# Kernel tuning notes

Measured on AMD Instinct MI355X. Metric: run time of the kernel, lower is better.

The kernel has to match this reference:

```python
import jax, jax.numpy as jnp
import numpy as np

N_NODES = 50000
N_EDGES = 800000
IN_CH = 64
HID = 128
OUT_CH = 1
NUM_LAYERS = 3
NUM_TIMESTEPS = 3
EDGE_DIM = 25
NUM_GRAPHS = 1024
NEG = 0.01  # leaky_relu negative slope (torch default & GATConv arg)


def leaky(v):
    return jnp.where(v >= 0, v, NEG * v)


def seg_softmax(a, idx, n):
    # PyG softmax: exp(a - max_per_segment) / (sum_per_segment + 1e-16)
    m = jax.ops.segment_max(a, idx, num_segments=n)
    m = jnp.where(jnp.isfinite(m), m, 0.0)  # guard empty segments
    e = jnp.exp(a - m[idx])
    s = jax.ops.segment_sum(e, idx, num_segments=n)
    return e / (s[idx] + 1e-16)


def gru(inp, h, Wih, Whh, bih, bhh):
    gi = inp @ Wih.T + bih
    gh = h @ Whh.T + bhh
    ir, iz, inn = jnp.split(gi, 3, axis=-1)
    hr, hz, hn = jnp.split(gh, 3, axis=-1)
    r = jax.nn.sigmoid(ir + hr)
    z = jax.nn.sigmoid(iz + hz)
    n = jnp.tanh(inn + r * hn)
    return (1.0 - z) * n + z * h


def setup_inputs() -> dict:
    key = jax.random.key(0)
    ks = iter(jax.random.split(key, 40))

    def nrm(shape, s=0.05):
        return jax.random.normal(next(ks), shape, dtype=jnp.float32) * s

    L = NUM_LAYERS - 1
    H3 = 3 * HID
    inp = dict(
        x=jax.random.normal(next(ks), (N_NODES, IN_CH), dtype=jnp.float32),
        edge_index=jax.random.randint(next(ks), (2, N_EDGES), 0, N_NODES),
        batch=jnp.sort(jax.random.randint(next(ks), (N_NODES,), 0, NUM_GRAPHS)),
        W1=nrm((HID, IN_CH)), b1=jnp.zeros((HID,), jnp.float32),
        Wg1=nrm((HID, HID + EDGE_DIM)), att_l=nrm((HID,)), att_r=nrm((HID,)),
        Wg2=nrm((HID, HID)), bg=jnp.zeros((HID,), jnp.float32),
        Wih0=nrm((H3, HID)), Whh0=nrm((H3, HID)),
        bih0=jnp.zeros((H3,), jnp.float32), bhh0=jnp.zeros((H3,), jnp.float32),
        Wa=nrm((L, HID, HID)), att_src_a=nrm((L, HID)), att_dst_a=nrm((L, HID)),
        ba=jnp.zeros((L, HID), jnp.float32),
        Wih_a=nrm((L, H3, HID)), Whh_a=nrm((L, H3, HID)),
        bih_a=jnp.zeros((L, H3), jnp.float32), bhh_a=jnp.zeros((L, H3), jnp.float32),
        Wm=nrm((HID, HID)), att_src_m=nrm((HID,)), att_dst_m=nrm((HID,)),
        bm=jnp.zeros((HID,), jnp.float32),
        Wih_m=nrm((H3, HID)), Whh_m=nrm((H3, HID)),
        bih_m=jnp.zeros((H3,), jnp.float32), bhh_m=jnp.zeros((H3,), jnp.float32),
        W2=nrm((OUT_CH, HID)), b2=jnp.zeros((OUT_CH,), jnp.float32),
    )
    return inp


def reference(x, edge_index, batch, W1, b1, Wg1, att_l, att_r, Wg2, bg,
              Wih0, Whh0, bih0, bhh0, Wa, att_src_a, att_dst_a, ba,
              Wih_a, Whh_a, bih_a, bhh_a, Wm, att_src_m, att_dst_m, bm,
              Wih_m, Whh_m, bih_m, bhh_m, W2, b2):
    N = x.shape[0]
    E = edge_index.shape[1]
    src, dst = edge_index[0], edge_index[1]  # j -> i, aggregate at i=dst
    edge_attr = jnp.ones((E, EDGE_DIM), dtype=x.dtype)  # built inside original forward

    x = leaky(x @ W1.T + b1)

    # GATEConv: edge-feature-aware attention, sum aggregation
    xe = leaky(jnp.concatenate([x[src], edge_attr], axis=-1) @ Wg1.T)  # [E, H]
    a = seg_softmax(leaky(xe @ att_l + (x @ att_r)[dst]), dst, N)
    msg = (x[src] @ Wg2.T) * a[:, None]
    h = jax.nn.elu(jax.ops.segment_sum(msg, dst, num_segments=N) + bg)
    x = jax.nn.relu(gru(h, x, Wih0, Whh0, bih0, bhh0))

    # (num_layers - 1) GATConv + GRU atom updates
    for l in range(NUM_LAYERS - 1):
        xt = x @ Wa[l].T
        a = seg_softmax(leaky((xt @ att_src_a[l])[src] + (xt @ att_dst_a[l])[dst]), dst, N)
        h = jax.nn.elu(jax.ops.segment_sum(xt[src] * a[:, None], dst, num_segments=N) + ba[l])
        x = jax.nn.relu(gru(h, x, Wih_a[l], Whh_a[l], bih_a[l], bhh_a[l]))

    # attentive readout: bipartite GATConv node->molecule over num_timesteps
    out = jax.nn.relu(jax.ops.segment_sum(x, batch, num_segments=NUM_GRAPHS))
    xt = x @ Wm.T                 # shared lin for src (fixed across timesteps)
    a_src = xt @ att_src_m        # [N]
    for _ in range(NUM_TIMESTEPS):
        ot = out @ Wm.T           # shared lin for dst
        a = seg_softmax(leaky(a_src + (ot @ att_dst_m)[batch]), batch, NUM_GRAPHS)
        h = jax.nn.elu(jax.ops.segment_sum(xt * a[:, None], batch, num_segments=NUM_GRAPHS) + bm)
        out = jax.nn.relu(gru(h, out, Wih_m, Whh_m, bih_m, bhh_m))

    return out @ W2.T + b2
```

## Files before the change

### kernel.cpp

```cpp
#include <hip/hip_runtime.h>
#include <math.h>

#define NN 50000
#define NE 800000
#define NG 1024
#define HID 128

typedef __attribute__((ext_vector_type(8))) short short8;
typedef __attribute__((ext_vector_type(4))) unsigned short ushort4v;
typedef __attribute__((ext_vector_type(4))) float f32x4;

__device__ __forceinline__ float leakyf(float v){ return v >= 0.f ? v : 0.01f*v; }
__device__ __forceinline__ float sigmf(float v){ return 1.f/(1.f+expf(-v)); }
__device__ __forceinline__ float eluf(float v){ return v > 0.f ? v : expm1f(v); }
__device__ __forceinline__ unsigned short bf16rne(float f){
  union { float f; unsigned u; } v; v.f = f;
  return (unsigned short)((v.u + 0x7FFFu + ((v.u >> 16) & 1u)) >> 16);
}
__device__ __forceinline__ float bf2f(unsigned short h){
  union { unsigned u; float f; } v; v.u = ((unsigned)h) << 16; return v.f;
}
__device__ __forceinline__ short8 cvt8(const float* a){
  short8 r;
#pragma unroll
  for (int j=0;j<8;j++) r[j] = (short)bf16rne(a[j]);
  return r;
}

__global__ __launch_bounds__(256)
void pack_all(const float* W1, const float* Wg1, const float* Wg2, const float* Wa,
              const float* Wm, const float* Wih0, const float* Whh0,
              const float* Wih_a, const float* Whh_a, const float* Wih_m,
              const float* Whh_m, unsigned short* __restrict__ dst)
{
  int m = (int)blockIdx.y;
  int t = (int)blockIdx.x*4 + ((int)threadIdx.x>>6);
  int l = (int)threadIdx.x & 63;
  const float* src; int stride=128, M=128, K=128; size_t doff;
  switch(m){
    case 0:  src=W1;    stride=64;  K=64;  doff=0;      break;
    case 1:  src=Wg1;   stride=153;        doff=8192;   break;
    case 2:  src=Wg2;                      doff=24576;  break;
    case 3:  src=Wa;                       doff=40960;  break;
    case 4:  src=Wa+16384;                 doff=57344;  break;
    case 5:  src=Wm;                       doff=73728;  break;
    case 6:  src=Wih0;  M=384;             doff=90112;  break;
    case 7:  src=Whh0;  M=384;             doff=139264; break;
    case 8:  src=Wih_a; M=384;             doff=188416; break;
    case 9:  src=Whh_a; M=384;             doff=237568; break;
    case 10: src=Wih_a+49152; M=384;       doff=286720; break;
    case 11: src=Whh_a+49152; M=384;       doff=335872; break;
    case 12: src=Wih_m; M=384;             doff=385024; break;
    default: src=Whh_m; M=384;             doff=434176; break;
  }
  int tk = K/32;
  if (t >= (M/16)*tk) return;
  int ct = t / tk, kc = t % tk;
  int row = ct*16 + (l&15);
  int col = kc*32 + ((l>>4)<<3);
  unsigned short o[8];
#pragma unroll
  for (int j=0;j<8;j++) o[j] = bf16rne(src[(size_t)row*stride + col + j]);
  ushort4v* d = (ushort4v*)(dst + doff + (((size_t)t*64 + l)<<3));
  ushort4v d0; d0.x=o[0]; d0.y=o[1]; d0.z=o[2]; d0.w=o[3];
  ushort4v d1; d1.x=o[4]; d1.y=o[5]; d1.z=o[6]; d1.w=o[7];
  d[0]=d0; d[1]=d1;
}

template<int K>
__global__ __launch_bounds__(256)
void gemm_direct(const float* __restrict__ A, const unsigned short* __restrict__ Wp,
                 const float* __restrict__ bias, float* __restrict__ Cf,
                 unsigned short* __restrict__ Cb,
                 const float* __restrict__ v1, const float* __restrict__ v2,
                 const float* __restrict__ va,
                 float* __restrict__ s1, float* __restrict__ s2, int rows, int act)
{
  __shared__ float sd1[2][32];
  __shared__ float sd2[2][32];
  constexpr int KC = K/32;
  const int tid=(int)threadIdx.x, w=tid>>6, l=tid&63;
  const int fr=l&15, fq=l>>4;
  const int rt=w>>1, ch=w&1;
  const int bn = (int)blockIdx.x*32;
  const int ar = bn + rt*16 + fr;
  f32x4 acc[4];
#pragma unroll
  for (int j=0;j<4;j++) acc[j] = (f32x4){0.f,0.f,0.f,0.f};
  float pa = 0.f;
#pragma unroll
  for (int kc=0;kc<KC;kc++){
    float a8[8];
    if (ar < rows){
      *(float4*)&a8[0] = *(const float4*)(A + (size_t)ar*K + kc*32 + fq*8);
      *(float4*)&a8[4] = *(const float4*)(A + (size_t)ar*K + kc*32 + fq*8 + 4);
    } else {
#pragma unroll
      for (int j=0;j<8;j++) a8[j]=0.f;
    }
    short8 fa = cvt8(a8);
    if (va && ch==0){
      float4 t0 = *(const float4*)(va + kc*32 + fq*8);
      float4 t1 = *(const float4*)(va + kc*32 + fq*8 + 4);
      pa += a8[0]*t0.x + a8[1]*t0.y + a8[2]*t0.z + a8[3]*t0.w
          + a8[4]*t1.x + a8[5]*t1.y + a8[6]*t1.z + a8[7]*t1.w;
    }
#pragma unroll
    for (int j=0;j<4;j++){
      const short8 bfr = *(const short8*)(Wp + ((((size_t)(ch*4+j)*KC + kc)*64 + l)<<3));
      acc[j] = __builtin_amdgcn_mfma_f32_16x16x32_bf16(fa, bfr, acc[j], 0, 0, 0);
    }
  }
  float dp1[4]={0.f,0.f,0.f,0.f}, dp2[4]={0.f,0.f,0.f,0.f};
#pragma unroll
  for (int j=0;j<4;j++){
    int c = ch*64 + j*16 + fr;
    float bv = bias ? bias[c] : 0.f;
    float w1 = v1 ? v1[c] : 0.f;
    float w2 = v2 ? v2[c] : 0.f;
#pragma unroll
    for (int r4=0;r4<4;r4++){
      float o = acc[j][r4] + bv;
      if (act) o = leakyf(o);
      dp1[r4] += o*w1; dp2[r4] += o*w2;
      int r = bn + rt*16 + fq*4 + r4;
      if (r < rows){
        if (Cf) Cf[(size_t)r*HID + c] = o;
        if (Cb) Cb[(size_t)r*HID + c] = bf16rne(o);
      }
    }
  }
  if (v1){
#pragma unroll
    for (int r4=0;r4<4;r4++){
#pragma unroll
      for (int m=1;m<16;m<<=1){ dp1[r4] += __shfl_xor(dp1[r4], m); dp2[r4] += __shfl_xor(dp2[r4], m); }
    }
    if (fr==0){
#pragma unroll
      for (int r4=0;r4<4;r4++){
        sd1[ch][rt*16 + fq*4 + r4] = dp1[r4];
        sd2[ch][rt*16 + fq*4 + r4] = dp2[r4];
      }
    }
    __syncthreads();
    if (tid < 32){
      int r = bn + tid;
      if (r < rows) s1[r] = sd1[0][tid] + sd1[1][tid];
    } else if (v2 && tid < 64){
      int r = bn + tid - 32;
      if (r < rows) s2[r] = sd2[0][tid-32] + sd2[1][tid-32];
    }
  }
  if (va && ch==0){
    pa += __shfl_xor(pa, 16); pa += __shfl_xor(pa, 32);
    if (fq==0){
      int r = bn + rt*16 + fr;
      if (r < rows) s2[r] = pa;
    }
  }
}

__global__ __launch_bounds__(256)
void fused_gru(const float* __restrict__ Ah, const float* __restrict__ Ax,
               const unsigned short* __restrict__ Wi, const unsigned short* __restrict__ Wh,
               const float* __restrict__ bih, const float* __restrict__ bhh,
               float* __restrict__ out, int rows)
{
  const int tid=(int)threadIdx.x, cq=tid>>6, l=tid&63;
  const int fr=l&15, fq=l>>4;
  const int bn = (int)blockIdx.x*16;
  const int ar = bn + fr;
  f32x4 ai[3][2], ah[3][2];
#pragma unroll
  for (int g=0;g<3;g++)
#pragma unroll
    for (int t=0;t<2;t++){ ai[g][t] = (f32x4){0,0,0,0}; ah[g][t] = (f32x4){0,0,0,0}; }
#pragma unroll
  for (int kc=0;kc<4;kc++){
    float a8[8], x8[8];
    if (ar < rows){
      *(float4*)&a8[0] = *(const float4*)(Ah + (size_t)ar*HID + kc*32 + fq*8);
      *(float4*)&a8[4] = *(const float4*)(Ah + (size_t)ar*HID + kc*32 + fq*8 + 4);
      *(float4*)&x8[0] = *(const float4*)(Ax + (size_t)ar*HID + kc*32 + fq*8);
      *(float4*)&x8[4] = *(const float4*)(Ax + (size_t)ar*HID + kc*32 + fq*8 + 4);
    } else {
#pragma unroll
      for (int j=0;j<8;j++){ a8[j]=0.f; x8[j]=0.f; }
    }
    short8 fa = cvt8(a8), fx = cvt8(x8);
#pragma unroll
    for (int g=0;g<3;g++)
#pragma unroll
      for (int t=0;t<2;t++){
        size_t woff = ((((size_t)(g*8 + cq*2 + t)*4 + kc)*64 + l)<<3);
        short8 wi = *(const short8*)(Wi + woff);
        short8 wh = *(const short8*)(Wh + woff);
        ai[g][t] = __builtin_amdgcn_mfma_f32_16x16x32_bf16(fa, wi, ai[g][t], 0, 0, 0);
        ah[g][t] = __builtin_amdgcn_mfma_f32_16x16x32_bf16(fx, wh, ah[g][t], 0, 0, 0);
      }
  }
#pragma unroll
  for (int t=0;t<2;t++){
    int c0 = (cq*2+t)*16 + fr;
    float bi_r=bih[c0], bi_z=bih[c0+128], bi_n=bih[c0+256];
    float bh_r=bhh[c0], bh_z=bhh[c0+128], bh_n=bhh[c0+256];
#pragma unroll
    for (int r4=0;r4<4;r4++){
      int row = bn + fq*4 + r4;
      if (row < rows){
        float rr = sigmf(ai[0][t][r4]+bi_r+ah[0][t][r4]+bh_r);
        float zz = sigmf(ai[1][t][r4]+bi_z+ah[1][t][r4]+bh_z);
        float nn = tanhf(ai[2][t][r4]+bi_n + rr*(ah[2][t][r4]+bh_n));
        float hv = Ax[(size_t)row*HID + c0];
        out[(size_t)row*HID + c0] = fmaxf((1.f-zz)*nn + zz*hv, 0.f);
      }
    }
  }
}

__global__ __launch_bounds__(256)
void rowdot(const float* __restrict__ A, const float* __restrict__ v,
            const float* __restrict__ bias, float* __restrict__ out, int rows)
{
  int wave = (int)((blockIdx.x * blockDim.x + threadIdx.x) >> 6);
  int lane = (int)(threadIdx.x & 63);
  if (wave >= rows) return;
  float2 a  = ((const float2*)(A + (size_t)wave*HID))[lane];
  float2 vv = ((const float2*)v)[lane];
  float s = a.x*vv.x + a.y*vv.y;
  for (int off=32; off; off>>=1) s += __shfl_down(s, off);
  if (lane==0) out[wave] = s + (bias ? bias[0] : 0.f);
}

__global__ void colvec(const float* __restrict__ W, const float* __restrict__ v,
                       float* __restrict__ out)
{
  int k = (int)threadIdx.x;
  float s = 0.f;
  for (int j=0;j<HID;j++) s += W[j*HID+k]*v[j];
  out[k] = s;
}

__global__ void prep_cg(const float* __restrict__ Wg1, float* __restrict__ cg){
  int j = (int)threadIdx.x;
  float s = 0.f;
  for (int k=128;k<153;k++) s += Wg1[j*153+k];
  cg[j] = s;
}

__global__ void count_kernel(const int* __restrict__ idx, int* __restrict__ cnt, int n){
  int i = (int)(blockIdx.x*blockDim.x + threadIdx.x);
  if (i < n) atomicAdd(&cnt[idx[i]], 1);
}

__global__ __launch_bounds__(1024)
void scan_blocks(const int* __restrict__ cnt, int* __restrict__ off,
                 int* __restrict__ tot, int n)
{
  __shared__ int buf[1024];
  int i = (int)(blockIdx.x*1024 + threadIdx.x);
  int v = (i<n)? cnt[i] : 0;
  buf[threadIdx.x] = v;
  __syncthreads();
  for (int s=1;s<1024;s<<=1){
    int t = ((int)threadIdx.x >= s) ? buf[threadIdx.x - s] : 0;
    __syncthreads();
    buf[threadIdx.x] += t;
    __syncthreads();
  }
  if (i<n) off[i] = buf[threadIdx.x] - v;
  if (threadIdx.x==1023) tot[blockIdx.x] = buf[1023];
}

__global__ void scan_tot(int* __restrict__ tot, int* __restrict__ off_end, int nb){
  int lane = (int)threadIdx.x;
  int orig = (lane<nb)? tot[lane] : 0;
  int v = orig;
  for (int s=1;s<64;s<<=1){ int t = __shfl_up(v, s); if (lane>=s) v += t; }
  int total = __shfl(v, 63);
  if (lane<nb) tot[lane] = v - orig;
  if (lane==0) *off_end = total;
}

__global__ void scan_add(int* __restrict__ off, const int* __restrict__ tot, int n){
  int i = (int)(blockIdx.x*blockDim.x + threadIdx.x);
  if (i<n) off[i] += tot[i>>10];
}

__global__ void fill_kernel(const int* __restrict__ src, const int* __restrict__ dst,
                            const int* __restrict__ off, int* __restrict__ fill,
                            int* __restrict__ ssrc, int n){
  int e = (int)(blockIdx.x*blockDim.x + threadIdx.x);
  if (e < n){
    int d = dst[e];
    int p = off[d] + atomicAdd(&fill[d], 1);
    ssrc[p] = src[e];
  }
}

__global__ void graph_bounds(const int* __restrict__ batch, int* __restrict__ goff){
  int g = (int)(blockIdx.x*blockDim.x + threadIdx.x);
  if (g > NG) return;
  int lo=0, hi=NN;
  while (lo<hi){ int mid=(lo+hi)>>1; if (batch[mid] < g) lo=mid+1; else hi=mid; }
  goff[g] = lo;
}

__global__ __launch_bounds__(256)
void agg_edges(const int* __restrict__ off, const int* __restrict__ ssrc,
               const float* __restrict__ ls, const float* __restrict__ ld,
               const unsigned short* __restrict__ Mrows, const float* __restrict__ bias,
               float* __restrict__ out, int n)
{
  __shared__ float wbuf[4][64];
  __shared__ int   sbuf[4][64];
  const int ws = (int)(threadIdx.x >> 6);
  int node = (int)((blockIdx.x * blockDim.x + threadIdx.x) >> 6);
  int lane = (int)(threadIdx.x & 63);
  if (node >= n) return;
  int e0 = off[node], e1 = off[node+1];
  float ldv = ld[node];
  const int h = lane >> 5, cl = lane & 31;
  float denom = 0.f;
  float4 acc = make_float4(0.f,0.f,0.f,0.f);
  for (int j0=e0; j0<e1; j0+=64){
    int cnt = min(64, e1-j0);
    float wv = 0.f; int sc = 0;
    if (lane < cnt){
      sc = ssrc[j0+lane];
      wv = expf(leakyf(ls[sc]+ldv));
    }
    denom += wv;
    wbuf[ws][lane] = wv;
    sbuf[ws][lane] = sc;
#pragma unroll 4
    for (int k2=0;k2<cnt;k2+=2){
      float wk = wbuf[ws][k2+h];
      int  sck = sbuf[ws][k2+h];
      uint2 mm = *(const uint2*)(Mrows + (size_t)sck*HID + cl*4);
      acc.x += wk*bf2f((unsigned short)(mm.x&0xffff));
      acc.y += wk*bf2f((unsigned short)(mm.x>>16));
      acc.z += wk*bf2f((unsigned short)(mm.y&0xffff));
      acc.w += wk*bf2f((unsigned short)(mm.y>>16));
    }
  }
  acc.x += __shfl_xor(acc.x, 32); acc.y += __shfl_xor(acc.y, 32);
  acc.z += __shfl_xor(acc.z, 32); acc.w += __shfl_xor(acc.w, 32);
  for (int o=32;o;o>>=1) denom += __shfl_xor(denom, o);
  if (h==0){
    float inv = 1.f/(denom + 1e-16f);
    float4 b = *(const float4*)(bias + cl*4);
    float4 o;
    o.x = eluf(acc.x*inv + b.x); o.y = eluf(acc.y*inv + b.y);
    o.z = eluf(acc.z*inv + b.z); o.w = eluf(acc.w*inv + b.w);
    *(float4*)(out + (size_t)node*HID + cl*4) = o;
  }
}

__global__ __launch_bounds__(256)
void graph_sum(const int* __restrict__ goff, const float* __restrict__ X,
               float* __restrict__ out)
{
  int g = (int)((blockIdx.x*blockDim.x + threadIdx.x) >> 6);
  int lane = (int)(threadIdx.x & 63);
  if (g >= NG) return;
  float2 acc = make_float2(0.f,0.f);
  for (int n=goff[g]; n<goff[g+1]; ++n){
    float2 v = ((const float2*)(X + (size_t)n*HID))[lane];
    acc.x += v.x; acc.y += v.y;
  }
  ((float2*)(out + (size_t)g*HID))[lane] = make_float2(fmaxf(acc.x,0.f), fmaxf(acc.y,0.f));
}

__global__ __launch_bounds__(256)
void graph_soft2(const int* __restrict__ goff, const float* __restrict__ asrc,
                 const float* __restrict__ gout, const float* __restrict__ vmd,
                 const unsigned short* __restrict__ Xt, const float* __restrict__ bias,
                 float* __restrict__ out)
{
  __shared__ float wbuf[4][64];
  const int ws = (int)(threadIdx.x >> 6);
  int g = (int)((blockIdx.x*blockDim.x + threadIdx.x) >> 6);
  int lane = (int)(threadIdx.x & 63);
  if (g >= NG) return;
  float2 ov = ((const float2*)(gout + (size_t)g*HID))[lane];
  float2 vv = ((const float2*)vmd)[lane];
  float ad = ov.x*vv.x + ov.y*vv.y;
  for (int o=32;o;o>>=1) ad += __shfl_xor(ad, o);
  int n0 = goff[g], n1 = goff[g+1];
  const int h = lane >> 5, cl = lane & 31;
  float denom = 0.f;
  float4 acc = make_float4(0.f,0.f,0.f,0.f);
  for (int j0=n0; j0<n1; j0+=64){
    int cnt = min(64, n1-j0);
    float wv = 0.f;
    if (lane < cnt) wv = expf(leakyf(asrc[j0+lane]+ad));
    denom += wv;
    wbuf[ws][lane] = wv;
#pragma unroll 4
    for (int k2=0;k2<cnt;k2+=2){
      float wk = wbuf[ws][k2+h];
      int rowi = min(j0 + k2 + h, n1 - 1);
      uint2 mm = *(const uint2*)(Xt + (size_t)rowi*HID + cl*4);
      acc.x += wk*bf2f((unsigned short)(mm.x&0xffff));
      acc.y += wk*bf2f((unsigned short)(mm.x>>16));
      acc.z += wk*bf2f((unsigned short)(mm.y&0xffff));
      acc.w += wk*bf2f((unsigned short)(mm.y>>16));
    }
  }
  acc.x += __shfl_xor(acc.x, 32); acc.y += __shfl_xor(acc.y, 32);
  acc.z += __shfl_xor(acc.z, 32); acc.w += __shfl_xor(acc.w, 32);
  for (int o=32;o;o>>=1) denom += __shfl_xor(denom, o);
  if (h==0){
    float inv = 1.f/(denom + 1e-16f);
    float4 b = *(const float4*)(bias + cl*4);
    float4 o;
    o.x = eluf(acc.x*inv + b.x); o.y = eluf(acc.y*inv + b.y);
    o.z = eluf(acc.z*inv + b.z); o.w = eluf(acc.w*inv + b.w);
    *(float4*)(out + (size_t)g*HID + cl*4) = o;
  }
}

extern "C" void kernel_launch(void* const* d_in, const int* in_sizes, int n_in,
                              void* d_out, int out_size, void* d_ws, size_t ws_size,
                              hipStream_t stream)
{
  const float* x_in  = (const float*)d_in[0];
  const int*   ei    = (const int*)d_in[1];
  const int*   batch = (const int*)d_in[2];
  const float* W1    = (const float*)d_in[3];
  const float* b1    = (const float*)d_in[4];
  const float* Wg1   = (const float*)d_in[5];
  const float* att_l = (const float*)d_in[6];
  const float* att_r = (const float*)d_in[7];
  const float* Wg2   = (const float*)d_in[8];
  const float* bg    = (const float*)d_in[9];
  const float* Wih0  = (const float*)d_in[10];
  const float* Whh0  = (const float*)d_in[11];
  const float* bih0  = (const float*)d_in[12];
  const float* bhh0  = (const float*)d_in[13];
  const float* Wa    = (const float*)d_in[14];
  const float* att_src_a = (const float*)d_in[15];
  const float* att_dst_a = (const float*)d_in[16];
  const float* ba    = (const float*)d_in[17];
  const float* Wih_a = (const float*)d_in[18];
  const float* Whh_a = (const float*)d_in[19];
  const float* bih_a = (const float*)d_in[20];
  const float* bhh_a = (const float*)d_in[21];
  const float* Wm    = (const float*)d_in[22];
  const float* att_src_m = (const float*)d_in[23];
  const float* att_dst_m = (const float*)d_in[24];
  const float* bm    = (const float*)d_in[25];
  const float* Wih_m = (const float*)d_in[26];
  const float* Whh_m = (const float*)d_in[27];
  const float* bih_m = (const float*)d_in[28];
  const float* bhh_m = (const float*)d_in[29];
  const float* W2    = (const float*)d_in[30];
  const float* b2    = (const float*)d_in[31];
  (void)in_sizes; (void)n_in; (void)out_size; (void)ws_size;

  char* wsb = (char*)d_ws;
  size_t off = 0;
  auto alloc = [&](size_t bytes)->void* {
    void* p = wsb + off;
    off += (bytes + 255) & ~(size_t)255;
    return p;
  };
  float* f_x   = (float*)alloc((size_t)NN*HID*4);
  float* f_xb  = (float*)alloc((size_t)NN*HID*4);
  float* f_h   = (float*)alloc((size_t)NN*HID*4);
  unsigned short* f_t = (unsigned short*)alloc((size_t)NN*HID*2);
  float* f_s1  = (float*)alloc((size_t)NN*4);
  float* f_s2  = (float*)alloc((size_t)NN*4);
  float* g_o0  = (float*)alloc((size_t)NG*HID*4);
  float* g_o1  = (float*)alloc((size_t)NG*HID*4);
  float* g_h   = (float*)alloc((size_t)NG*HID*4);
  float* w_cg  = (float*)alloc((size_t)HID*4);
  float* w_vmd = (float*)alloc((size_t)HID*4);
  unsigned short* w_pack = (unsigned short*)alloc((size_t)483328*2);
  int* i_cnt   = (int*)alloc((size_t)NN*4);
  int* i_off   = (int*)alloc((size_t)(NN+1)*4);
  int* i_fill  = (int*)alloc((size_t)NN*4);
  int* i_src   = (int*)alloc((size_t)NE*4);
  int* i_tot   = (int*)alloc((size_t)64*4);
  int* i_goff  = (int*)alloc((size_t)(NG+1)*4);

  const unsigned short* pk_W1   = w_pack + 0;
  const unsigned short* pk_g1   = w_pack + 8192;
  const unsigned short* pk_g2   = w_pack + 24576;
  const unsigned short* pk_wa0  = w_pack + 40960;
  const unsigned short* pk_wa1  = w_pack + 57344;
  const unsigned short* pk_wm   = w_pack + 73728;
  const unsigned short* pk_wih0 = w_pack + 90112;
  const unsigned short* pk_whh0 = w_pack + 139264;
  const unsigned short* pk_wiha0= w_pack + 188416;
  const unsigned short* pk_whha0= w_pack + 237568;
  const unsigned short* pk_wiha1= w_pack + 286720;
  const unsigned short* pk_whha1= w_pack + 335872;
  const unsigned short* pk_wihm = w_pack + 385024;
  const unsigned short* pk_whhm = w_pack + 434176;

  const int* e_src = ei;
  const int* e_dst = ei + NE;

  hipMemsetAsync(i_cnt, 0, (size_t)NN*4, stream);
  hipMemsetAsync(i_fill, 0, (size_t)NN*4, stream);

  const int NB = (NN + 1023)/1024;
  count_kernel<<<(NE+255)/256,256,0,stream>>>(e_dst, i_cnt, NE);
  scan_blocks<<<NB,1024,0,stream>>>(i_cnt, i_off, i_tot, NN);
  scan_tot<<<1,64,0,stream>>>(i_tot, i_off+NN, NB);
  scan_add<<<(NN+255)/256,256,0,stream>>>(i_off, i_tot, NN);
  fill_kernel<<<(NE+255)/256,256,0,stream>>>(e_src, e_dst, i_off, i_fill, i_src, NE);
  graph_bounds<<<(NG+1+255)/256,256,0,stream>>>(batch, i_goff);
  prep_cg<<<1,128,0,stream>>>(Wg1, w_cg);
  colvec<<<1,128,0,stream>>>(Wm, att_dst_m, w_vmd);
  pack_all<<<dim3(24,14),256,0,stream>>>(W1, Wg1, Wg2, Wa, Wm, Wih0, Whh0,
                                         Wih_a, Whh_a, Wih_m, Whh_m, w_pack);

  const int GB = (NN+31)/32;
  const int FB = (NN+15)/16;
  const int wavegrid_g = (NG*64)/256;

  gemm_direct<64><<<GB,256,0,stream>>>(x_in, pk_W1, b1, f_x, nullptr,
                                       nullptr,nullptr,nullptr,nullptr,nullptr, NN, 1);

  float* cur = f_x;
  float* nxt = f_xb;

  gemm_direct<128><<<GB,256,0,stream>>>(cur, pk_g1, w_cg, nullptr, nullptr,
                                        att_l, nullptr, att_r, f_s1, f_s2, NN, 1);
  gemm_direct<128><<<GB,256,0,stream>>>(cur, pk_g2, nullptr, nullptr, f_t,
                                        nullptr,nullptr,nullptr,nullptr,nullptr, NN, 0);
  agg_edges<<<(NN+3)/4,256,0,stream>>>(i_off, i_src, f_s1, f_s2, f_t, bg, f_h, NN);
  fused_gru<<<FB,256,0,stream>>>(f_h, cur, pk_wih0, pk_whh0, bih0, bhh0, nxt, NN);
  { float* t=cur; cur=nxt; nxt=t; }

  for (int l=0;l<2;l++){
    gemm_direct<128><<<GB,256,0,stream>>>(cur, l ? pk_wa1 : pk_wa0, nullptr, nullptr, f_t,
                                          att_src_a + l*HID, att_dst_a + l*HID, nullptr,
                                          f_s1, f_s2, NN, 0);
    agg_edges<<<(NN+3)/4,256,0,stream>>>(i_off, i_src, f_s1, f_s2, f_t, ba + l*HID, f_h, NN);
    fused_gru<<<FB,256,0,stream>>>(f_h, cur,
                                   l ? pk_wiha1 : pk_wiha0, l ? pk_whha1 : pk_whha0,
                                   bih_a + l*384, bhh_a + l*384, nxt, NN);
    { float* t=cur; cur=nxt; nxt=t; }
  }

  graph_sum<<<wavegrid_g,256,0,stream>>>(i_goff, cur, g_o0);
  gemm_direct<128><<<GB,256,0,stream>>>(cur, pk_wm, nullptr, nullptr, f_t,
                                        att_src_m, nullptr, nullptr, f_s1, nullptr, NN, 0);
  float* gc = g_o0; float* gn = g_o1;
  for (int t=0;t<3;t++){
    graph_soft2<<<wavegrid_g,256,0,stream>>>(i_goff, f_s1, gc, w_vmd, f_t, bm, g_h);
    fused_gru<<<(NG+15)/16,256,0,stream>>>(g_h, gc, pk_wihm, pk_whhm, bih_m, bhh_m, gn, NG);
    { float* tt=gc; gc=gn; gn=tt; }
  }

  rowdot<<<wavegrid_g,256,0,stream>>>(gc, W2, b2, (float*)d_out, NG);
}
```

Measured before the change: 663.0 us.

## Keep bf16 activation copies and restructure GRU to hold weights in registers

Node features are now written in both fp32 and bf16, so the GEMMs and the GRU read bf16 activations directly instead of loading fp32 and converting. The aggregation output is stored as bf16 only. fused_gru now uses 512-thread blocks, each wave keeping its weight fragments in registers across 8 row tiles, which cuts repeated weight loads. In exchange there are extra bf16 stores and heavy register pressure. The GRU also drops its row bounds check and relies on NN and NG being multiples of 16.

```diff
diff --git a/kernel.cpp b/kernel.cpp
--- a/kernel.cpp
+++ b/kernel.cpp
@@ -67,18 +67,12 @@
   d[0]=d0; d[1]=d1;
 }
 
-template<int K>
 __global__ __launch_bounds__(256)
-void gemm_direct(const float* __restrict__ A, const unsigned short* __restrict__ Wp,
-                 const float* __restrict__ bias, float* __restrict__ Cf,
-                 unsigned short* __restrict__ Cb,
-                 const float* __restrict__ v1, const float* __restrict__ v2,
-                 const float* __restrict__ va,
-                 float* __restrict__ s1, float* __restrict__ s2, int rows, int act)
-{
-  __shared__ float sd1[2][32];
-  __shared__ float sd2[2][32];
-  constexpr int KC = K/32;
+void gemm_f32(const float* __restrict__ A, const unsigned short* __restrict__ Wp,
+              const float* __restrict__ bias, float* __restrict__ Cf,
+              unsigned short* __restrict__ Cb, int rows, int act)
+{
+  constexpr int K = 64, KC = 2;
   const int tid=(int)threadIdx.x, w=tid>>6, l=tid&63;
   const int fr=l&15, fq=l>>4;
   const int rt=w>>1, ch=w&1;
@@ -87,7 +81,6 @@
   f32x4 acc[4];
 #pragma unroll
   for (int j=0;j<4;j++) acc[j] = (f32x4){0.f,0.f,0.f,0.f};
-  float pa = 0.f;
 #pragma unroll
   for (int kc=0;kc<KC;kc++){
     float a8[8];
@@ -99,11 +92,60 @@
       for (int j=0;j<8;j++) a8[j]=0.f;
     }
     short8 fa = cvt8(a8);
+#pragma unroll
+    for (int j=0;j<4;j++){
+      const short8 bfr = *(const short8*)(Wp + ((((size_t)(ch*4+j)*KC + kc)*64 + l)<<3));
+      acc[j] = __builtin_amdgcn_mfma_f32_16x16x32_bf16(fa, bfr, acc[j], 0, 0, 0);
+    }
+  }
+#pragma unroll
+  for (int j=0;j<4;j++){
+    int c = ch*64 + j*16 + fr;
+    float bv = bias ? bias[c] : 0.f;
+#pragma unroll
+    for (int r4=0;r4<4;r4++){
+      float o = acc[j][r4] + bv;
+      if (act) o = leakyf(o);
+      int r = bn + rt*16 + fq*4 + r4;
+      if (r < rows){
+        Cf[(size_t)r*HID + c] = o;
+        Cb[(size_t)r*HID + c] = bf16rne(o);
+      }
+    }
+  }
+}
+
+__global__ __launch_bounds__(256)
+void gemm_b16(const unsigned short* __restrict__ Ab, const unsigned short* __restrict__ Wp,
+              const float* __restrict__ bias, unsigned short* __restrict__ Cb,
+              const float* __restrict__ v1, const float* __restrict__ v2,
+              const float* __restrict__ va,
+              float* __restrict__ s1, float* __restrict__ s2, int rows, int act)
+{
+  __shared__ float sd1[2][32];
+  __shared__ float sd2[2][32];
+  constexpr int KC = 4;
+  const int tid=(int)threadIdx.x, w=tid>>6, l=tid&63;
+  const int fr=l&15, fq=l>>4;
+  const int rt=w>>1, ch=w&1;
+  const int bn = (int)blockIdx.x*32;
+  const int ar = bn + rt*16 + fr;
+  f32x4 acc[4];
+#pragma unroll
+  for (int j=0;j<4;j++) acc[j] = (f32x4){0.f,0.f,0.f,0.f};
+  float pa = 0.f;
+#pragma unroll
+  for (int kc=0;kc<KC;kc++){
+    short8 fa;
+    if (ar < rows) fa = *(const short8*)(Ab + (size_t)ar*HID + kc*32 + fq*8);
+    else { short8 z = {0,0,0,0,0,0,0,0}; fa = z; }
     if (va && ch==0){
       float4 t0 = *(const float4*)(va + kc*32 + fq*8);
       float4 t1 = *(const float4*)(va + kc*32 + fq*8 + 4);
-      pa += a8[0]*t0.x + a8[1]*t0.y + a8[2]*t0.z + a8[3]*t0.w
-          + a8[4]*t1.x + a8[5]*t1.y + a8[6]*t1.z + a8[7]*t1.w;
+      pa += bf2f((unsigned short)fa[0])*t0.x + bf2f((unsigned short)fa[1])*t0.y
+          + bf2f((unsigned short)fa[2])*t0.z + bf2f((unsigned short)fa[3])*t0.w
+          + bf2f((unsigned short)fa[4])*t1.x + bf2f((unsigned short)fa[5])*t1.y
+          + bf2f((unsigned short)fa[6])*t1.z + bf2f((unsigned short)fa[7])*t1.w;
     }
 #pragma unroll
     for (int j=0;j<4;j++){
@@ -124,10 +166,7 @@
       if (act) o = leakyf(o);
       dp1[r4] += o*w1; dp2[r4] += o*w2;
       int r = bn + rt*16 + fq*4 + r4;
-      if (r < rows){
-        if (Cf) Cf[(size_t)r*HID + c] = o;
-        if (Cb) Cb[(size_t)r*HID + c] = bf16rne(o);
-      }
+      if (r < rows && Cb) Cb[(size_t)r*HID + c] = bf16rne(o);
     }
   }
   if (v1){
@@ -161,60 +200,55 @@
   }
 }
 
-__global__ __launch_bounds__(256)
-void fused_gru(const float* __restrict__ Ah, const float* __restrict__ Ax,
+__global__ __launch_bounds__(512, 2)
+void fused_gru(const unsigned short* __restrict__ Ahb, const unsigned short* __restrict__ Axb,
+               const float* __restrict__ Axf,
                const unsigned short* __restrict__ Wi, const unsigned short* __restrict__ Wh,
                const float* __restrict__ bih, const float* __restrict__ bhh,
-               float* __restrict__ out, int rows)
-{
-  const int tid=(int)threadIdx.x, cq=tid>>6, l=tid&63;
+               float* __restrict__ outf, unsigned short* __restrict__ outb, int tiles)
+{
+  const int tid=(int)threadIdx.x, w=tid>>6, l=tid&63;
   const int fr=l&15, fq=l>>4;
-  const int bn = (int)blockIdx.x*16;
-  const int ar = bn + fr;
-  f32x4 ai[3][2], ah[3][2];
+  short8 wi_r[3][4], wh_r[3][4];
 #pragma unroll
   for (int g=0;g<3;g++)
 #pragma unroll
-    for (int t=0;t<2;t++){ ai[g][t] = (f32x4){0,0,0,0}; ah[g][t] = (f32x4){0,0,0,0}; }
-#pragma unroll
-  for (int kc=0;kc<4;kc++){
-    float a8[8], x8[8];
-    if (ar < rows){
-      *(float4*)&a8[0] = *(const float4*)(Ah + (size_t)ar*HID + kc*32 + fq*8);
-      *(float4*)&a8[4] = *(const float4*)(Ah + (size_t)ar*HID + kc*32 + fq*8 + 4);
-      *(float4*)&x8[0] = *(const float4*)(Ax + (size_t)ar*HID + kc*32 + fq*8);
-      *(float4*)&x8[4] = *(const float4*)(Ax + (size_t)ar*HID + kc*32 + fq*8 + 4);
-    } else {
-#pragma unroll
-      for (int j=0;j<8;j++){ a8[j]=0.f; x8[j]=0.f; }
-    }
-    short8 fa = cvt8(a8), fx = cvt8(x8);
-#pragma unroll
-    for (int g=0;g<3;g++)
-#pragma unroll
-      for (int t=0;t<2;t++){
-        size_t woff = ((((size_t)(g*8 + cq*2 + t)*4 + kc)*64 + l)<<3);
-        short8 wi = *(const short8*)(Wi + woff);
-        short8 wh = *(const short8*)(Wh + woff);
-        ai[g][t] = __builtin_amdgcn_mfma_f32_16x16x32_bf16(fa, wi, ai[g][t], 0, 0, 0);
-        ah[g][t] = __builtin_amdgcn_mfma_f32_16x16x32_bf16(fx, wh, ah[g][t], 0, 0, 0);
-      }
-  }
-#pragma unroll
-  for (int t=0;t<2;t++){
-    int c0 = (cq*2+t)*16 + fr;
-    float bi_r=bih[c0], bi_z=bih[c0+128], bi_n=bih[c0+256];
-    float bh_r=bhh[c0], bh_z=bhh[c0+128], bh_n=bhh[c0+256];
+    for (int kc=0;kc<4;kc++){
+      size_t o = ((((size_t)(g*8 + w)*4 + kc)*64 + l)<<3);
+      wi_r[g][kc] = *(const short8*)(Wi + o);
+      wh_r[g][kc] = *(const short8*)(Wh + o);
+    }
+  const int c0 = w*16 + fr;
+  float bi0=bih[c0], bi1=bih[c0+128], bi2=bih[c0+256];
+  float bh0=bhh[c0], bh1=bhh[c0+128], bh2=bhh[c0+256];
+
+  int rt_end = min((int)blockIdx.x*8 + 8, tiles);
+  for (int rt = (int)blockIdx.x*8; rt < rt_end; rt++){
+    const int bn = rt*16;
+    const int arow = bn + fr;
+    f32x4 ai0={0,0,0,0}, ai1={0,0,0,0}, ai2={0,0,0,0};
+    f32x4 ah0={0,0,0,0}, ah1={0,0,0,0}, ah2={0,0,0,0};
+#pragma unroll
+    for (int kc=0;kc<4;kc++){
+      short8 fa = *(const short8*)(Ahb + (size_t)arow*HID + kc*32 + fq*8);
+      short8 fx = *(const short8*)(Axb + (size_t)arow*HID + kc*32 + fq*8);
+      ai0 = __builtin_amdgcn_mfma_f32_16x16x32_bf16(fa, wi_r[0][kc], ai0, 0, 0, 0);
+      ai1 = __builtin_amdgcn_mfma_f32_16x16x32_bf16(fa, wi_r[1][kc], ai1, 0, 0, 0);
+      ai2 = __builtin_amdgcn_mfma_f32_16x16x32_bf16(fa, wi_r[2][kc], ai2, 0, 0, 0);
+      ah0 = __builtin_amdgcn_mfma_f32_16x16x32_bf16(fx, wh_r[0][kc], ah0, 0, 0, 0);
+      ah1 = __builtin_amdgcn_mfma_f32_16x16x32_bf16(fx, wh_r[1][kc], ah1, 0, 0, 0);
+      ah2 = __builtin_amdgcn_mfma_f32_16x16x32_bf16(fx, wh_r[2][kc], ah2, 0, 0, 0);
+    }
 #pragma unroll
     for (int r4=0;r4<4;r4++){
       int row = bn + fq*4 + r4;
-      if (row < rows){
-        float rr = sigmf(ai[0][t][r4]+bi_r+ah[0][t][r4]+bh_r);
-        float zz = sigmf(ai[1][t][r4]+bi_z+ah[1][t][r4]+bh_z);
-        float nn = tanhf(ai[2][t][r4]+bi_n + rr*(ah[2][t][r4]+bh_n));
-        float hv = Ax[(size_t)row*HID + c0];
-        out[(size_t)row*HID + c0] = fmaxf((1.f-zz)*nn + zz*hv, 0.f);
-      }
+      float rr = sigmf(ai0[r4] + bi0 + ah0[r4] + bh0);
+      float zz = sigmf(ai1[r4] + bi1 + ah1[r4] + bh1);
+      float nn = tanhf(ai2[r4] + bi2 + rr*(ah2[r4] + bh2));
+      float hv = Axf[(size_t)row*HID + c0];
+      float o = fmaxf((1.f - zz)*nn + zz*hv, 0.f);
+      outf[(size_t)row*HID + c0] = o;
+      outb[(size_t)row*HID + c0] = bf16rne(o);
     }
   }
 }
@@ -311,7 +345,7 @@
 void agg_edges(const int* __restrict__ off, const int* __restrict__ ssrc,
                const float* __restrict__ ls, const float* __restrict__ ld,
                const unsigned short* __restrict__ Mrows, const float* __restrict__ bias,
-               float* __restrict__ out, int n)
+               unsigned short* __restrict__ outb, int n)
 {
   __shared__ float wbuf[4][64];
   __shared__ int   sbuf[4][64];
@@ -351,16 +385,18 @@
   if (h==0){
     float inv = 1.f/(denom + 1e-16f);
     float4 b = *(const float4*)(bias + cl*4);
-    float4 o;
-    o.x = eluf(acc.x*inv + b.x); o.y = eluf(acc.y*inv + b.y);
-    o.z = eluf(acc.z*inv + b.z); o.w = eluf(acc.w*inv + b.w);
-    *(float4*)(out + (size_t)node*HID + cl*4) = o;
+    ushort4v ob;
+    ob.x = bf16rne(eluf(acc.x*inv + b.x));
+    ob.y = bf16rne(eluf(acc.y*inv + b.y));
+    ob.z = bf16rne(eluf(acc.z*inv + b.z));
+    ob.w = bf16rne(eluf(acc.w*inv + b.w));
+    *(ushort4v*)(outb + (size_t)node*HID + cl*4) = ob;
   }
 }
 
 __global__ __launch_bounds__(256)
 void graph_sum(const int* __restrict__ goff, const float* __restrict__ X,
-               float* __restrict__ out)
+               float* __restrict__ outf, unsigned short* __restrict__ outb)
 {
   int g = (int)((blockIdx.x*blockDim.x + threadIdx.x) >> 6);
   int lane = (int)(threadIdx.x & 63);
@@ -370,14 +406,17 @@
     float2 v = ((const float2*)(X + (size_t)n*HID))[lane];
     acc.x += v.x; acc.y += v.y;
   }
-  ((float2*)(out + (size_t)g*HID))[lane] = make_float2(fmaxf(acc.x,0.f), fmaxf(acc.y,0.f));
+  float ox = fmaxf(acc.x,0.f), oy = fmaxf(acc.y,0.f);
+  ((float2*)(outf + (size_t)g*HID))[lane] = make_float2(ox, oy);
+  unsigned u = (unsigned)bf16rne(ox) | ((unsigned)bf16rne(oy) << 16);
+  *(unsigned*)(outb + (size_t)g*HID + lane*2) = u;
 }
 
 __global__ __launch_bounds__(256)
 void graph_soft2(const int* __restrict__ goff, const float* __restrict__ asrc,
                  const float* __restrict__ gout, const float* __restrict__ vmd,
                  const unsigned short* __restrict__ Xt, const float* __restrict__ bias,
-                 float* __restrict__ out)
+                 unsigned short* __restrict__ outb)
 {
   __shared__ float wbuf[4][64];
   const int ws = (int)(threadIdx.x >> 6);
@@ -415,10 +454,12 @@
   if (h==0){
     float inv = 1.f/(denom + 1e-16f);
     float4 b = *(const float4*)(bias + cl*4);
-    float4 o;
-    o.x = eluf(acc.x*inv + b.x); o.y = eluf(acc.y*inv + b.y);
-    o.z = eluf(acc.z*inv + b.z); o.w = eluf(acc.w*inv + b.w);
-    *(float4*)(out + (size_t)g*HID + cl*4) = o;
+    ushort4v ob;
+    ob.x = bf16rne(eluf(acc.x*inv + b.x));
+    ob.y = bf16rne(eluf(acc.y*inv + b.y));
+    ob.z = bf16rne(eluf(acc.z*inv + b.z));
+    ob.w = bf16rne(eluf(acc.w*inv + b.w));
+    *(ushort4v*)(outb + (size_t)g*HID + cl*4) = ob;
   }
 }
 
@@ -468,14 +509,18 @@
     return p;
   };
   float* f_x   = (float*)alloc((size_t)NN*HID*4);
-  float* f_xb  = (float*)alloc((size_t)NN*HID*4);
-  float* f_h   = (float*)alloc((size_t)NN*HID*4);
-  unsigned short* f_t = (unsigned short*)alloc((size_t)NN*HID*2);
+  float* f_y   = (float*)alloc((size_t)NN*HID*4);
+  unsigned short* f_xb = (unsigned short*)alloc((size_t)NN*HID*2);
+  unsigned short* f_yb = (unsigned short*)alloc((size_t)NN*HID*2);
+  unsigned short* f_h  = (unsigned short*)alloc((size_t)NN*HID*2);
+  unsigned short* f_t  = (unsigned short*)alloc((size_t)NN*HID*2);
   float* f_s1  = (float*)alloc((size_t)NN*4);
   float* f_s2  = (float*)alloc((size_t)NN*4);
-  float* g_o0  = (float*)alloc((size_t)NG*HID*4);
-  float* g_o1  = (float*)alloc((size_t)NG*HID*4);
-  float* g_h   = (float*)alloc((size_t)NG*HID*4);
+  float* g_of0 = (float*)alloc((size_t)NG*HID*4);
+  float* g_of1 = (float*)alloc((size_t)NG*HID*4);
+  unsigned short* g_ob0 = (unsigned short*)alloc((size_t)NG*HID*2);
+  unsigned short* g_ob1 = (unsigned short*)alloc((size_t)NG*HID*2);
+  unsigned short* g_hb  = (unsigned short*)alloc((size_t)NG*HID*2);
   float* w_cg  = (float*)alloc((size_t)HID*4);
   float* w_vmd = (float*)alloc((size_t)HID*4);
   unsigned short* w_pack = (unsigned short*)alloc((size_t)483328*2);
@@ -520,43 +565,47 @@
                                          Wih_a, Whh_a, Wih_m, Whh_m, w_pack);
 
   const int GB = (NN+31)/32;
-  const int FB = (NN+15)/16;
+  const int NT = NN/16;
+  const int FB = (NT+7)/8;
+  const int GT = NG/16;
   const int wavegrid_g = (NG*64)/256;
 
-  gemm_direct<64><<<GB,256,0,stream>>>(x_in, pk_W1, b1, f_x, nullptr,
-                                       nullptr,nullptr,nullptr,nullptr,nullptr, NN, 1);
-
-  float* cur = f_x;
-  float* nxt = f_xb;
-
-  gemm_direct<128><<<GB,256,0,stream>>>(cur, pk_g1, w_cg, nullptr, nullptr,
-                                        att_l, nullptr, att_r, f_s1, f_s2, NN, 1);
-  gemm_direct<128><<<GB,256,0,stream>>>(cur, pk_g2, nullptr, nullptr, f_t,
-                                        nullptr,nullptr,nullptr,nullptr,nullptr, NN, 0);
+  gemm_f32<<<GB,256,0,stream>>>(x_in, pk_W1, b1, f_x, f_xb, NN, 1);
+
+  float* curf = f_x;  unsigned short* curb = f_xb;
+  float* nxtf = f_y;  unsigned short* nxtb = f_yb;
+
+  gemm_b16<<<GB,256,0,stream>>>(curb, pk_g1, w_cg, nullptr,
+                                att_l, nullptr, att_r, f_s1, f_s2, NN, 1);
+  gemm_b16<<<GB,256,0,stream>>>(curb, pk_g2, nullptr, f_t,
+                                nullptr,nullptr,nullptr,nullptr,nullptr, NN, 0);
   agg_edges<<<(NN+3)/4,256,0,stream>>>(i_off, i_src, f_s1, f_s2, f_t, bg, f_h, NN);
-  fused_gru<<<FB,256,0,stream>>>(f_h, cur, pk_wih0, pk_whh0, bih0, bhh0, nxt, NN);
-  { float* t=cur; cur=nxt; nxt=t; }
+  fused_gru<<<FB,512,0,stream>>>(f_h, curb, curf, pk_wih0, pk_whh0, bih0, bhh0,
+                                 nxtf, nxtb, NT);
+  { float* t=curf; curf=nxtf; nxtf=t; unsigned short* tb=curb; curb=nxtb; nxtb=tb; }
 
   for (int l=0;l<2;l++){
-    gemm_direct<128><<<GB,256,0,stream>>>(cur, l ? pk_wa1 : pk_wa0, nullptr, nullptr, f_t,
-                                          att_src_a + l*HID, att_dst_a + l*HID, nullptr,
-                                          f_s1, f_s2, NN, 0);
+    gemm_b16<<<GB,256,0,stream>>>(curb, l ? pk_wa1 : pk_wa0, nullptr, f_t,
+                                  att_src_a + l*HID, att_dst_a + l*HID, nullptr,
+                                  f_s1, f_s2, NN, 0);
     agg_edges<<<(NN+3)/4,256,0,stream>>>(i_off, i_src, f_s1, f_s2, f_t, ba + l*HID, f_h, NN);
-    fused_gru<<<FB,256,0,stream>>>(f_h, cur,
+    fused_gru<<<FB,512,0,stream>>>(f_h, curb, curf,
                                    l ? pk_wiha1 : pk_wiha0, l ? pk_whha1 : pk_whha0,
-                                   bih_a + l*384, bhh_a + l*384, nxt, NN);
-    { float* t=cur; cur=nxt; nxt=t; }
-  }
-
-  graph_sum<<<wavegrid_g,256,0,stream>>>(i_goff, cur, g_o0);
-  gemm_direct<128><<<GB,256,0,stream>>>(cur, pk_wm, nullptr, nullptr, f_t,
-                                        att_src_m, nullptr, nullptr, f_s1, nullptr, NN, 0);
-  float* gc = g_o0; float* gn = g_o1;
+                                   bih_a + l*384, bhh_a + l*384, nxtf, nxtb, NT);
+    { float* t=curf; curf=nxtf; nxtf=t; unsigned short* tb=curb; curb=nxtb; nxtb=tb; }
+  }
+
+  graph_sum<<<wavegrid_g,256,0,stream>>>(i_goff, curf, g_of0, g_ob0);
+  gemm_b16<<<GB,256,0,stream>>>(curb, pk_wm, nullptr, f_t,
+                                att_src_m, nullptr, nullptr, f_s1, nullptr, NN, 0);
+  float* gcf = g_of0; unsigned short* gcb = g_ob0;
+  float* gnf = g_of1; unsigned short* gnb = g_ob1;
   for (int t=0;t<3;t++){
-    graph_soft2<<<wavegrid_g,256,0,stream>>>(i_goff, f_s1, gc, w_vmd, f_t, bm, g_h);
-    fused_gru<<<(NG+15)/16,256,0,stream>>>(g_h, gc, pk_wihm, pk_whhm, bih_m, bhh_m, gn, NG);
-    { float* tt=gc; gc=gn; gn=tt; }
-  }
-
-  rowdot<<<wavegrid_g,256,0,stream>>>(gc, W2, b2, (float*)d_out, NG);
-}
+    graph_soft2<<<wavegrid_g,256,0,stream>>>(i_goff, f_s1, gcf, w_vmd, f_t, bm, g_hb);
+    fused_gru<<<(GT+7)/8,512,0,stream>>>(g_hb, gcb, gcf, pk_wihm, pk_whhm,
+                                         bih_m, bhh_m, gnf, gnb, GT);
+    { float* tf=gcf; gcf=gnf; gnf=tf; unsigned short* tb=gcb; gcb=gnb; gnb=tb; }
+  }
+
+  rowdot<<<wavegrid_g,256,0,stream>>>(gcf, W2, b2, (float*)d_out, NG);
+}
```

After: 664.5 us. No clear change (+0.2%).
